# Performance work log

Hardware: AMD Instinct MI355X
Metric: run time of the kernel (lower is better)

Reference implementation:

```python
import jax, jax.numpy as jnp
import numpy as np

N_HOPS = 2
NEG_SLOPE = 0.2


def setup_inputs() -> dict:
    key = jax.random.key(0)
    k1, k2, k3, k4, k5 = jax.random.split(key, 5)
    N, E, D, R = 100000, 1600000, 64, 64
    edge_index = jax.random.randint(k1, (2, E), 0, N, dtype=jnp.int64)
    edge_type = jax.random.randint(k2, (E,), 0, R, dtype=jnp.int64)
    entity_emb = jax.random.normal(k3, (N, D), dtype=jnp.float32) * 0.1
    relation_emb = jax.random.normal(k4, (R, D), dtype=jnp.float32) * 0.1
    W = jax.random.normal(k5, (2 * D, D), dtype=jnp.float32) * 0.1
    return {"edge_index": edge_index, "edge_type": edge_type,
            "entity_emb": entity_emb, "relation_emb": relation_emb, "W": W}


def _hop(emb, head, tail, rel_e, W, N):
    # gather head/tail embeddings: [E, 2D]
    a_input = jnp.concatenate([emb[head], emb[tail]], axis=-1)
    # relation-gated attention logit per edge: [E]
    e = jnp.sum((a_input @ W) * rel_e, axis=-1)
    e = jax.nn.leaky_relu(e, NEG_SLOPE)
    # scatter-softmax grouped by head node
    seg_max = jax.ops.segment_max(e, head, num_segments=N)  # [N]
    ex = jnp.exp(e - seg_max[head])
    denom = jax.ops.segment_sum(ex, head, num_segments=N)   # [N]
    alpha = ex / denom[head]
    # weighted scatter-sum aggregation + residual
    agg = jax.ops.segment_sum(emb[tail] * alpha[:, None], head, num_segments=N)
    return agg + emb


def reference(edge_index, edge_type, entity_emb, relation_emb, W):
    head, tail = edge_index[0], edge_index[1]
    N = entity_emb.shape[0]
    rel_e = relation_emb[edge_type]  # [E, D], constant across hops
    res = entity_emb
    emb = entity_emb
    for _ in range(N_HOPS):
        emb = _hop(emb, head, tail, rel_e, W, N)
        # F.normalize: row-wise L2 with eps 1e-12 (dropout disabled)
        norm = jnp.maximum(jnp.linalg.norm(emb, axis=-1, keepdims=True), 1e-12)
        emb = emb / norm
        res = 0.5 * res + emb
    return res
```

## Files before the change

### kernel.cpp

```cpp
#include <hip/hip_runtime.h>


#define NEG_SLOPE 0.2f
#define CAP 64
#define BKT_SHIFT 8
#define BKT_CAP 6144

__device__ __forceinline__ float b2f_lo(unsigned x) {
    return __uint_as_float(x << 16);
}
__device__ __forceinline__ float b2f_hi(unsigned x) {
    return __uint_as_float(x & 0xffff0000u);
}
__device__ __forceinline__ unsigned short f2b(float x) {
    unsigned u = __float_as_uint(x);
    unsigned r = u + 0x7fffu + ((u >> 16) & 1u);
    return (unsigned short)(r >> 16);
}

__device__ __forceinline__ float dot2bf(unsigned a, unsigned b, float c) {
    float d;
    asm("v_dot2_f32_bf16 %0, %1, %2, %3" : "=v"(d) : "v"(a), "v"(b), "v"(c));
    return d;
}

__device__ __forceinline__ float ror_sum16(float x) {
#define ROR_ADD(ctrl)                                                          \
    x += __int_as_float(                                                       \
        __builtin_amdgcn_update_dpp(0, __float_as_int(x), ctrl, 0xf, 0xf, true))
    ROR_ADD(0x121);
    ROR_ADD(0x122);
    ROR_ADD(0x124);
    ROR_ADD(0x128);
#undef ROR_ADD
    return x;
}

__global__ __launch_bounds__(256) void init_kernel(
    const float* __restrict__ W, const float* __restrict__ rel,
    unsigned short* __restrict__ Wuvb, const float* __restrict__ ent,
    unsigned short* __restrict__ entb, int* __restrict__ gcursor,
    int n4, int R, int nbkt) {
    if ((int)blockIdx.x < R) {
        int r = blockIdx.x;
        int i = threadIdx.x;
        __shared__ float rels[64];
        if (i < 64) rels[i] = rel[r * 64 + i];
        __syncthreads();
        if (i < 128) {
            float s = 0.f;
#pragma unroll
            for (int j = 0; j < 64; ++j) s += W[i * 64 + j] * rels[j];
            int d = i & 63, half = i >> 6;
            Wuvb[r * 128 + (d >> 2) * 8 + half * 4 + (d & 3)] = f2b(s);
        }
    } else if ((int)blockIdx.x == R) {
        for (int i = threadIdx.x; i < nbkt; i += 256) gcursor[i] = 0;
    } else {
        int i = (blockIdx.x - R - 1) * 256 + threadIdx.x;
        if (i < n4) {
            float4 v = *(const float4*)(ent + (long)i * 4);
            ushort4 o = {f2b(v.x), f2b(v.y), f2b(v.z), f2b(v.w)};
            *(ushort4*)(entb + (long)i * 4) = o;
        }
    }
}

__global__ __launch_bounds__(256) void binA_kernel(
    const int* __restrict__ head, const int* __restrict__ tail,
    const int* __restrict__ etype, int* __restrict__ gcursor,
    uint2* __restrict__ stream, int E, int nbkt) {
    __shared__ int lcnt[512];
    __shared__ int lbase[512];
    int nb = gridDim.x;
    long e0 = (long)blockIdx.x * E / nb;
    long e1 = (long)(blockIdx.x + 1) * E / nb;
    for (int i = threadIdx.x; i < nbkt; i += 256) lcnt[i] = 0;
    __syncthreads();
    for (long i = e0 + threadIdx.x; i < e1; i += 256)
        atomicAdd(&lcnt[head[i] >> BKT_SHIFT], 1);
    __syncthreads();
    for (int b = threadIdx.x; b < nbkt; b += 256) {
        lbase[b] = atomicAdd(gcursor + b, lcnt[b]);
        lcnt[b] = 0;
    }
    __syncthreads();
    for (long i = e0 + threadIdx.x; i < e1; i += 256) {
        int h = head[i];
        int b = h >> BKT_SHIFT;
        int entry = (tail[i] << 6) | etype[i];
        int p = lbase[b] + atomicAdd(&lcnt[b], 1);
        if (p < BKT_CAP)
            stream[(long)b * BKT_CAP + p] = make_uint2((unsigned)h, (unsigned)entry);
    }
}

__global__ __launch_bounds__(256) void binB_kernel(
    const int* __restrict__ gcursor, const uint2* __restrict__ stream,
    int* __restrict__ deg, int* __restrict__ csr, int N) {
    __shared__ int cnt[256];
    int b = blockIdx.x;
    cnt[threadIdx.x] = 0;
    __syncthreads();
    int n = min(gcursor[b], BKT_CAP);
    const uint2* sp = stream + (long)b * BKT_CAP;
    for (int i = threadIdx.x; i < n; i += 256) {
        uint2 e = sp[i];
        int c = atomicAdd(&cnt[e.x & 255], 1);
        if (c < CAP) csr[(long)e.x * CAP + c] = (int)e.y;
    }
    __syncthreads();
    int node = (b << BKT_SHIFT) + threadIdx.x;
    if (node < N) deg[node] = cnt[threadIdx.x];
}

__global__ __launch_bounds__(512) void hop_kernel(
    const int* __restrict__ degp, const int* __restrict__ csr,
    const unsigned short* __restrict__ Wuvb,
    const unsigned short* __restrict__ embb, const float* res_prev,
    unsigned short* embb_out, float* res_out, int N) {
    __shared__ unsigned short sUV[64 * 136];
    for (int k = threadIdx.x; k < 64 * 128; k += 512) {
        int r = k >> 7, q = k & 127;
        sUV[r * 136 + q] = Wuvb[k];
    }
    __syncthreads();

    int tid = threadIdx.x;
    int s = tid & 15;
    int node = blockIdx.x * 32 + (tid >> 4);
    bool valid = node < N;
    long nb64 = (long)node * 64;

    uint2 hdp = valid ? *(const uint2*)(embb + nb64 + s * 4)
                      : make_uint2(0u, 0u);

    int deg = valid ? min(degp[node], CAP) : 0;
    int r0 = node * CAP;
    int dmin = min(min(__shfl(deg, 0), __shfl(deg, 16)),
                   min(__shfl(deg, 32), __shfl(deg, 48)));
    int dmax = max(max(__shfl(deg, 0), __shfl(deg, 16)),
                   max(__shfl(deg, 32), __shfl(deg, 48)));

    float a0 = 0.f, a1 = 0.f, a2 = 0.f, a3 = 0.f, l = 0.f;

    auto edge_body = [&](int pe, uint2 rw, bool gated, int idx) {
        int rr = pe & 63;
        uint4 uv = *(const uint4*)(sUV + rr * 136 + s * 8);
        float sd = dot2bf(hdp.x, uv.x, 0.f);
        sd = dot2bf(hdp.y, uv.y, sd);
        sd = dot2bf(rw.x, uv.z, sd);
        sd = dot2bf(rw.y, uv.w, sd);
        sd = ror_sum16(sd);
        float p = fmaxf(sd, NEG_SLOPE * sd);
        float w = __expf(p);
        if (gated) w = (idx < deg) ? w : 0.f;
        l += w;
        float e0 = b2f_lo(rw.x), e1 = b2f_hi(rw.x);
        float e2 = b2f_lo(rw.y), e3 = b2f_hi(rw.y);
        a0 += w * e0; a1 += w * e1; a2 += w * e2; a3 += w * e3;
    };

    int c = 0;
    for (; c + 8 <= dmin; c += 8) {
        uint4 ea = *(const uint4*)(csr + r0 + c);
        uint4 eb = *(const uint4*)(csr + r0 + c + 4);
        int pe[8] = {(int)ea.x, (int)ea.y, (int)ea.z, (int)ea.w,
                     (int)eb.x, (int)eb.y, (int)eb.z, (int)eb.w};
        uint2 rw[8];
#pragma unroll
        for (int u = 0; u < 8; ++u)
            rw[u] = *(const uint2*)(embb + (long)(pe[u] >> 6) * 64 + s * 4);
#pragma unroll
        for (int u = 0; u < 8; ++u) edge_body(pe[u], rw[u], false, 0);
    }
    for (; c < dmax; c += 4) {
        uint4 e4 = *(const uint4*)(csr + r0 + c);
        int pe[4];
        pe[0] = (c + 0 < deg) ? (int)e4.x : 0;
        pe[1] = (c + 1 < deg) ? (int)e4.y : 0;
        pe[2] = (c + 2 < deg) ? (int)e4.z : 0;
        pe[3] = (c + 3 < deg) ? (int)e4.w : 0;
        uint2 rw[4];
#pragma unroll
        for (int u = 0; u < 4; ++u)
            rw[u] = *(const uint2*)(embb + (long)(pe[u] >> 6) * 64 + s * 4);
#pragma unroll
        for (int u = 0; u < 4; ++u) edge_body(pe[u], rw[u], true, c + u);
    }

    if (valid) {
        float hd0 = b2f_lo(hdp.x), hd1 = b2f_hi(hdp.x);
        float hd2 = b2f_lo(hdp.y), hd3 = b2f_hi(hdp.y);
        float inv = (l > 0.f) ? 1.f / l : 0.f;
        float v0 = hd0 + a0 * inv, v1 = hd1 + a1 * inv;
        float v2 = hd2 + a2 * inv, v3 = hd3 + a3 * inv;
        float sq = v0 * v0 + v1 * v1 + v2 * v2 + v3 * v3;
        sq = ror_sum16(sq);
        float rn = 1.f / fmaxf(sqrtf(sq), 1e-12f);
        v0 *= rn; v1 *= rn; v2 *= rn; v3 *= rn;
        if (embb_out) {
            ushort4 o = {f2b(v0), f2b(v1), f2b(v2), f2b(v3)};
            *(ushort4*)(embb_out + nb64 + s * 4) = o;
        }
        float4 rp = *(const float4*)(res_prev + nb64 + s * 4);
        float4 ro = {0.5f * rp.x + v0, 0.5f * rp.y + v1,
                     0.5f * rp.z + v2, 0.5f * rp.w + v3};
        *(float4*)(res_out + nb64 + s * 4) = ro;
    }
}

extern "C" void kernel_launch(void* const* d_in, const int* in_sizes, int n_in,
                              void* d_out, int out_size, void* d_ws, size_t ws_size,
                              hipStream_t stream) {
    const int*   edge_index = (const int*)d_in[0];
    const int*   etype      = (const int*)d_in[1];
    const float* ent        = (const float*)d_in[2];
    const float* rel        = (const float*)d_in[3];
    const float* W          = (const float*)d_in[4];

    const int E = in_sizes[1];
    const int N = in_sizes[2] / 64;
    const int R = in_sizes[3] / 64;
    const int* head = edge_index;
    const int* tail = edge_index + E;
    float* out = (float*)d_out;

    const int nbkt = ((N - 1) >> BKT_SHIFT) + 1;

    char* w = (char*)d_ws;
    unsigned short* Wuvb = (unsigned short*)w;  w += (size_t)R * 128 * 2;
    int* gcursor = (int*)w;                     w += 512 * 4;
    int* deg = (int*)w;                         w += ((size_t)N + 64) * 4;
    int* csr = (int*)w;                         w += (size_t)N * CAP * 4;
    uint2* bstream = (uint2*)w;                 w += (size_t)nbkt * BKT_CAP * 8;
    unsigned short* entb = (unsigned short*)w;  w += (size_t)N * 64 * 2;
    unsigned short* emb1b = (unsigned short*)w; w += (size_t)N * 64 * 2;

    const int n4 = N * 16;
    const int ib = R + 1 + (n4 + 255) / 256;
    const int hb = (N + 31) / 32;

    init_kernel<<<ib, 256, 0, stream>>>(W, rel, Wuvb, ent, entb, gcursor,
                                        n4, R, nbkt);

    binA_kernel<<<512, 256, 0, stream>>>(head, tail, etype, gcursor,
                                         bstream, E, nbkt);
    binB_kernel<<<nbkt, 256, 0, stream>>>(gcursor, bstream, deg, csr, N);

    hop_kernel<<<hb, 512, 0, stream>>>(deg, csr, Wuvb, entb, ent, emb1b, out, N);
    hop_kernel<<<hb, 512, 0, stream>>>(deg, csr, Wuvb, emb1b, out, nullptr, out, N);
}
```

Baseline: 265.0 us.

## Sort nodes by degree within buckets and stage CSR writes through shared memory

Bucket size is halved to 128 nodes. binB now builds each bucket's CSR rows in LDS and writes them out coalesced, 16 lanes per row. It also computes a per-bucket permutation that orders nodes by degree, which the hop kernel uses so the 4 nodes sharing a wavefront have similar degrees and dmin/dmax divergence shrinks. A 4-wide ungated loop is added between the 8-wide loop and the gated tail. The cost is an extra perm lookup and the loss of locality between consecutive node IDs in each hop.

```diff
diff --git a/kernel.cpp b/kernel.cpp
--- a/kernel.cpp
+++ b/kernel.cpp
@@ -3,8 +3,8 @@
 
 #define NEG_SLOPE 0.2f
 #define CAP 64
-#define BKT_SHIFT 8
-#define BKT_CAP 6144
+#define BKT_SHIFT 7
+#define BKT_CAP 3072
 
 __device__ __forceinline__ float b2f_lo(unsigned x) {
     return __uint_as_float(x << 16);
@@ -70,8 +70,8 @@
     const int* __restrict__ head, const int* __restrict__ tail,
     const int* __restrict__ etype, int* __restrict__ gcursor,
     uint2* __restrict__ stream, int E, int nbkt) {
-    __shared__ int lcnt[512];
-    __shared__ int lbase[512];
+    __shared__ int lcnt[1024];
+    __shared__ int lbase[1024];
     int nb = gridDim.x;
     long e0 = (long)blockIdx.x * E / nb;
     long e1 = (long)(blockIdx.x + 1) * E / nb;
@@ -97,25 +97,59 @@
 
 __global__ __launch_bounds__(256) void binB_kernel(
     const int* __restrict__ gcursor, const uint2* __restrict__ stream,
-    int* __restrict__ deg, int* __restrict__ csr, int N) {
-    __shared__ int cnt[256];
+    int* __restrict__ deg, int* __restrict__ csr, int* __restrict__ perm,
+    int N) {
+    __shared__ int cnt[128];
+    __shared__ int hist[CAP + 2];
+    __shared__ unsigned csrS[128 * 65];
     int b = blockIdx.x;
-    cnt[threadIdx.x] = 0;
+    if (threadIdx.x < 128) cnt[threadIdx.x] = 0;
+    if (threadIdx.x < CAP + 2) hist[threadIdx.x] = 0;
     __syncthreads();
     int n = min(gcursor[b], BKT_CAP);
     const uint2* sp = stream + (long)b * BKT_CAP;
     for (int i = threadIdx.x; i < n; i += 256) {
         uint2 e = sp[i];
-        int c = atomicAdd(&cnt[e.x & 255], 1);
-        if (c < CAP) csr[(long)e.x * CAP + c] = (int)e.y;
-    }
-    __syncthreads();
-    int node = (b << BKT_SHIFT) + threadIdx.x;
-    if (node < N) deg[node] = cnt[threadIdx.x];
+        int l = e.x & 127;
+        int c = atomicAdd(&cnt[l], 1);
+        if (c < CAP) csrS[l * 65 + c] = e.y;
+    }
+    __syncthreads();
+    int l = threadIdx.x, d = 0, rank = 0;
+    bool v = false;
+    if (l < 128) {
+        int node = (b << BKT_SHIFT) + l;
+        v = node < N;
+        if (v) {
+            deg[node] = cnt[l];
+            d = min(cnt[l], CAP);
+            rank = atomicAdd(&hist[d], 1);
+        }
+    }
+    __syncthreads();
+    if (threadIdx.x == 0) {
+        int s = 0;
+        for (int i = 0; i <= CAP; ++i) { int t = hist[i]; hist[i] = s; s += t; }
+    }
+    __syncthreads();
+    if (v) perm[(b << BKT_SHIFT) + hist[d] + rank] = (b << BKT_SHIFT) + l;
+    int w4 = threadIdx.x >> 6, lane = threadIdx.x & 63;
+    int q = lane >> 4, sL = lane & 15;
+    for (int j = 0; j < 8; ++j) {
+        int ln = ((j & 3) << 5) + (q << 3) + ((j >> 2) << 2) + w4;
+        int node = (b << BKT_SHIFT) + ln;
+        if (node < N) {
+            int dcl = min(cnt[ln], CAP);
+            for (int r = 0; r * 16 < dcl; ++r)
+                csr[(long)node * CAP + r * 16 + sL] =
+                    (int)csrS[ln * 65 + r * 16 + sL];
+        }
+    }
 }
 
 __global__ __launch_bounds__(512) void hop_kernel(
     const int* __restrict__ degp, const int* __restrict__ csr,
+    const int* __restrict__ perm,
     const unsigned short* __restrict__ Wuvb,
     const unsigned short* __restrict__ embb, const float* res_prev,
     unsigned short* embb_out, float* res_out, int N) {
@@ -128,8 +162,9 @@
 
     int tid = threadIdx.x;
     int s = tid & 15;
-    int node = blockIdx.x * 32 + (tid >> 4);
-    bool valid = node < N;
+    int gi = blockIdx.x * 32 + (tid >> 4);
+    bool valid = gi < N;
+    int node = valid ? perm[gi] : 0;
     long nb64 = (long)node * 64;
 
     uint2 hdp = valid ? *(const uint2*)(embb + nb64 + s * 4)
@@ -174,6 +209,16 @@
 #pragma unroll
         for (int u = 0; u < 8; ++u) edge_body(pe[u], rw[u], false, 0);
     }
+    for (; c + 4 <= dmin; c += 4) {
+        uint4 e4 = *(const uint4*)(csr + r0 + c);
+        int pe[4] = {(int)e4.x, (int)e4.y, (int)e4.z, (int)e4.w};
+        uint2 rw[4];
+#pragma unroll
+        for (int u = 0; u < 4; ++u)
+            rw[u] = *(const uint2*)(embb + (long)(pe[u] >> 6) * 64 + s * 4);
+#pragma unroll
+        for (int u = 0; u < 4; ++u) edge_body(pe[u], rw[u], false, 0);
+    }
     for (; c < dmax; c += 4) {
         uint4 e4 = *(const uint4*)(csr + r0 + c);
         int pe[4];
@@ -230,12 +275,13 @@
 
     char* w = (char*)d_ws;
     unsigned short* Wuvb = (unsigned short*)w;  w += (size_t)R * 128 * 2;
-    int* gcursor = (int*)w;                     w += 512 * 4;
+    int* gcursor = (int*)w;                     w += 1024 * 4;
     int* deg = (int*)w;                         w += ((size_t)N + 64) * 4;
     int* csr = (int*)w;                         w += (size_t)N * CAP * 4;
     uint2* bstream = (uint2*)w;                 w += (size_t)nbkt * BKT_CAP * 8;
     unsigned short* entb = (unsigned short*)w;  w += (size_t)N * 64 * 2;
     unsigned short* emb1b = (unsigned short*)w; w += (size_t)N * 64 * 2;
+    int* perm = (int*)w;                        w += ((size_t)N + 64) * 4;
 
     const int n4 = N * 16;
     const int ib = R + 1 + (n4 + 255) / 256;
@@ -246,8 +292,10 @@
 
     binA_kernel<<<512, 256, 0, stream>>>(head, tail, etype, gcursor,
                                          bstream, E, nbkt);
-    binB_kernel<<<nbkt, 256, 0, stream>>>(gcursor, bstream, deg, csr, N);
-
-    hop_kernel<<<hb, 512, 0, stream>>>(deg, csr, Wuvb, entb, ent, emb1b, out, N);
-    hop_kernel<<<hb, 512, 0, stream>>>(deg, csr, Wuvb, emb1b, out, nullptr, out, N);
-}
+    binB_kernel<<<nbkt, 256, 0, stream>>>(gcursor, bstream, deg, csr, perm, N);
+
+    hop_kernel<<<hb, 512, 0, stream>>>(deg, csr, perm, Wuvb, entb, ent,
+                                       emb1b, out, N);
+    hop_kernel<<<hb, 512, 0, stream>>>(deg, csr, perm, Wuvb, emb1b, out,
+                                       nullptr, out, N);
+}
```

Result: faster. 247.8 us (-6.5%).
